# Kernel tuning notes

Measured on AMD Instinct MI355X. Metric: run time of the kernel, lower is better.

Reference implementation:

```python
import jax, jax.numpy as jnp
import numpy as np

DIM = 96
GROUPS = 8          # SPPE factor
CG = DIM // GROUPS  # channels per SPPE group = 12
D_STATE = 16
D_CONV = 4
D_INNER = 2 * DIM   # expand=2
DT_RANK = 6         # ceil(96/16)
EPS = 1e-5


def setup_inputs() -> dict:
    key = jax.random.key(0)
    ks = jax.random.split(key, 16)
    def w(k, shape, s=0.02):
        return (jax.random.normal(k, shape) * s).astype(jnp.float32)
    z = lambda *s: jnp.zeros(s, jnp.float32)
    inp = {
        "x": jax.random.normal(ks[0], (2, DIM, 32, 32, 32), dtype=jnp.float32),
        # SPPE params
        "sppe_c1_w": w(ks[1], (CG, CG)), "sppe_c1_b": z(CG),
        "sppe_c3_w": w(ks[2], (CG, CG, 3, 3, 3)), "sppe_c3_b": z(CG),
        "sppe_gn_w": jnp.ones((CG,), jnp.float32), "sppe_gn_b": z(CG),
        # Mamba params (mamba_ssm defaults: proj biases False, conv bias True)
        "in_proj_w": w(ks[3], (2 * D_INNER, DIM)),
        "conv1d_w": w(ks[4], (D_INNER, D_CONV), 0.1), "conv1d_b": z(D_INNER),
        "x_proj_w": w(ks[5], (DT_RANK + 2 * D_STATE, D_INNER)),
        "dt_proj_w": w(ks[6], (D_INNER, DT_RANK), 0.1),
        "dt_proj_b": w(ks[7], (D_INNER,), 0.1),
        "A_log": jnp.log(jnp.tile(jnp.arange(1, D_STATE + 1, dtype=jnp.float32), (D_INNER, 1))),
        "ssm_D": jnp.ones((D_INNER,), jnp.float32),
        "out_proj_w": w(ks[8], (DIM, D_INNER)),
        # MlpChannel params (1x1 Conv3d == pointwise linear over channels)
        "mlp_fc1_w": w(ks[9], (4 * DIM, DIM)), "mlp_fc1_b": z(4 * DIM),
        "mlp_fc2_w": w(ks[10], (DIM, 4 * DIM)), "mlp_fc2_b": z(DIM),
    }
    return inp


def _inorm(x):
    # InstanceNorm3d (affine=False, biased var) over spatial dims per (b,c)
    m = jnp.mean(x, axis=(2, 3, 4), keepdims=True)
    v = jnp.var(x, axis=(2, 3, 4), keepdims=True)
    return (x - m) * jax.lax.rsqrt(v + EPS)


def _sppe(x, c1_w, c1_b, c3_w, c3_b, gn_w, gn_b):
    b, c, h, w, d = x.shape
    bg = b * GROUPS
    gx = x.reshape(bg, CG, h, w, d)
    # directional pools, each ending as (bg, CG, axis_len, 1, 1)
    x_h = jnp.mean(gx, axis=(3, 4), keepdims=True)                      # (bg,CG,h,1,1)
    x_w = jnp.mean(gx, axis=(2, 4), keepdims=True).transpose(0, 1, 3, 2, 4)
    x_d = jnp.mean(gx, axis=(2, 3), keepdims=True).transpose(0, 1, 4, 3, 2)
    hwd = jnp.concatenate([x_h, x_w, x_d], axis=2)[..., 0, 0]          # (bg,CG,h+w+d)
    hwd = jnp.einsum("oc,bcn->bon", c1_w, hwd) + c1_b[:, None]
    g_h = jax.nn.sigmoid(hwd[:, :, :h])[:, :, :, None, None]           # (bg,CG,h,1,1)
    g_w = jax.nn.sigmoid(hwd[:, :, h:h + w])[:, :, None, :, None]      # (bg,CG,1,w,1)
    g_d = jax.nn.sigmoid(hwd[:, :, h + w:])[:, :, None, None, :]       # (bg,CG,1,1,d)
    gated = gx * g_h * g_w * g_d
    # GroupNorm(num_groups=CG, num_channels=CG) == per-channel norm + affine
    gm = jnp.mean(gated, axis=(2, 3, 4), keepdims=True)
    gv = jnp.var(gated, axis=(2, 3, 4), keepdims=True)
    x1 = (gated - gm) * jax.lax.rsqrt(gv + EPS)
    x1 = x1 * gn_w[:, None, None, None] + gn_b[:, None, None, None]
    x2 = jax.lax.conv_general_dilated(
        gx, c3_w, (1, 1, 1), [(1, 1)] * 3,
        dimension_numbers=("NCDHW", "OIDHW", "NCDHW")) + c3_b[:, None, None, None]
    n = h * w * d
    x11 = jax.nn.softmax(jnp.mean(x1, axis=(2, 3, 4)), axis=-1)        # (bg,CG)
    x21 = jax.nn.softmax(jnp.mean(x2, axis=(2, 3, 4)), axis=-1)
    x12 = x2.reshape(bg, CG, n)
    x22 = x1.reshape(bg, CG, n)
    weights = (jnp.einsum("bc,bcn->bn", x11, x12)
               + jnp.einsum("bc,bcn->bn", x21, x22)).reshape(bg, 1, h, w, d)
    return (gx * jax.nn.sigmoid(weights)).reshape(b, c, h, w, d)


def _mamba(seq, in_proj_w, conv1d_w, conv1d_b, x_proj_w, dt_proj_w, dt_proj_b,
           A_log, ssm_D, out_proj_w):
    # seq: (B, L, DIM)
    B, L, _ = seq.shape
    xz = seq @ in_proj_w.T                       # (B,L,2*E)
    xm, zg = jnp.split(xz, 2, axis=-1)
    # depthwise causal conv1d along L
    xc = jax.lax.conv_general_dilated(
        xm.transpose(0, 2, 1), conv1d_w[:, None, :], (1,), [(D_CONV - 1, 0)],
        dimension_numbers=("NCH", "OIH", "NCH"), feature_group_count=D_INNER)
    xc = jax.nn.silu((xc + conv1d_b[:, None]).transpose(0, 2, 1))  # (B,L,E)
    dbl = xc @ x_proj_w.T                         # (B,L,DT_RANK+2N)
    dt = jax.nn.softplus(dbl[..., :DT_RANK] @ dt_proj_w.T + dt_proj_b)  # (B,L,E)
    Bm = dbl[..., DT_RANK:DT_RANK + D_STATE]      # (B,L,N)
    Cm = dbl[..., DT_RANK + D_STATE:]             # (B,L,N)
    A = -jnp.exp(A_log)                           # (E,N)

    def step(h, t):
        dt_t, b_t, c_t, x_t = t                   # (B,E),(B,N),(B,N),(B,E)
        dA = jnp.exp(dt_t[:, :, None] * A)        # (B,E,N)
        h = h * dA + (dt_t * x_t)[:, :, None] * b_t[:, None, :]
        return h, jnp.einsum("ben,bn->be", h, c_t)

    h0 = jnp.zeros((B, D_INNER, D_STATE), seq.dtype)
    _, ys = jax.lax.scan(step, h0, (dt.transpose(1, 0, 2), Bm.transpose(1, 0, 2),
                                    Cm.transpose(1, 0, 2), xc.transpose(1, 0, 2)))
    y = ys.transpose(1, 0, 2) + xc * ssm_D
    y = y * jax.nn.silu(zg)
    return y @ out_proj_w.T                       # (B,L,DIM)


def reference(x, sppe_c1_w, sppe_c1_b, sppe_c3_w, sppe_c3_b, sppe_gn_w, sppe_gn_b,
              in_proj_w, conv1d_w, conv1d_b, x_proj_w, dt_proj_w, dt_proj_b,
              A_log, ssm_D, out_proj_w, mlp_fc1_w, mlp_fc1_b, mlp_fc2_w, mlp_fc2_b):
    y_sppe = _sppe(x, sppe_c1_w, sppe_c1_b, sppe_c3_w, sppe_c3_b, sppe_gn_w, sppe_gn_b)
    B, C, H, W, Dd = x.shape
    L = H * W * Dd
    seq = _inorm(x).reshape(B, C, L).transpose(0, 2, 1)           # (B,L,C)
    out = _mamba(seq, in_proj_w, conv1d_w, conv1d_b, x_proj_w,
                 dt_proj_w, dt_proj_b, A_log, ssm_D, out_proj_w)
    xo = out.transpose(0, 2, 1).reshape(B, C, H, W, Dd)
    xo = _inorm(xo) * y_sppe
    t = jnp.einsum("oc,bchwd->bohwd", mlp_fc1_w, xo) + mlp_fc1_b[:, None, None, None]
    t = jax.nn.gelu(t, approximate=False)
    t = jnp.einsum("oc,bchwd->bohwd", mlp_fc2_w, t) + mlp_fc2_b[:, None, None, None]
    return t + x
```

## Files before the change

kernel.cpp:

```cpp
#include <hip/hip_runtime.h>
#include <math.h>

#define NSPA 32768
#define TCH 32
#define NCH 1024
#define EPS 1e-5f

#define ST_MEAN   0
#define ST_RSTD   192
#define ST_GM     384
#define ST_GRSTD  576
#define ST_X2SUM  768
#define ST_XH     1024
#define ST_XW     7168
#define ST_XD     13312
#define ST_GATE   19456
#define ST_MEAN2  38400
#define ST_RSTD2  38592
#define ST_WT     40960

__device__ __forceinline__ float sigmoidf_(float x){ return 1.f/(1.f+__expf(-x)); }
__device__ __forceinline__ float siluf_(float x){ return x/(1.f+__expf(-x)); }
__device__ __forceinline__ float geluf_(float x){ return 0.5f*x*(1.f+erff(x*0.70710678118654752f)); }
__device__ __forceinline__ float softplusf_(float x){ return fmaxf(x,0.f) + log1pf(__expf(-fabsf(x))); }

__global__ void k_stats(const float* __restrict__ x, float* __restrict__ st) {
  int bc = blockIdx.x;
  int t = threadIdx.x;
  __shared__ float xh_s[32], xw_s[32], xd_s[32], red[16], red2[16];
  if (t < 32) { xh_s[t]=0.f; xw_s[t]=0.f; xd_s[t]=0.f; }
  __syncthreads();
  const float* px = x + (size_t)bc*NSPA;
  float s=0.f, s2=0.f;
  for (int it=0; it<32; ++it) {
    float v = px[it*1024 + t];
    s += v; s2 += v*v;
    float wv = v;
    #pragma unroll
    for (int m=32;m>=1;m>>=1) wv += __shfl_xor(wv,m);
    if ((t&63)==0) atomicAdd(&xh_s[it], wv);
  }
  atomicAdd(&xw_s[(t>>5)&31], s);
  atomicAdd(&xd_s[t&31], s);
  float rs=s, rs2=s2;
  #pragma unroll
  for (int m=32;m>=1;m>>=1){ rs += __shfl_xor(rs,m); rs2 += __shfl_xor(rs2,m); }
  if ((t&63)==0){ red[t>>6]=rs; red2[t>>6]=rs2; }
  __syncthreads();
  if (t==0){
    float S=0.f,S2=0.f;
    for (int w=0;w<16;w++){ S+=red[w]; S2+=red2[w]; }
    float mn = S/(float)NSPA;
    float var = S2/(float)NSPA - mn*mn;
    st[ST_MEAN+bc] = mn;
    st[ST_RSTD+bc] = rsqrtf(var+EPS);
  }
  if (t<32){
    st[ST_XH + bc*32 + t] = xh_s[t]*(1.f/1024.f);
    st[ST_XW + bc*32 + t] = xw_s[t]*(1.f/1024.f);
    st[ST_XD + bc*32 + t] = xd_s[t]*(1.f/1024.f);
  }
}

__global__ void k_gates(const float* __restrict__ c1w, const float* __restrict__ c1b,
                        float* __restrict__ st) {
  int bg = blockIdx.x; int b = bg>>3; int g = bg&7;
  for (int i = threadIdx.x; i < 12*96; i += 128) {
    int co = i/96, pos = i%96;
    float acc = c1b[co];
    for (int cg=0; cg<12; ++cg) {
      int bc = b*96 + g*12 + cg;
      float hv;
      if (pos < 32)      hv = st[ST_XH + bc*32 + pos];
      else if (pos < 64) hv = st[ST_XW + bc*32 + pos-32];
      else               hv = st[ST_XD + bc*32 + pos-64];
      acc += c1w[co*12+cg]*hv;
    }
    st[ST_GATE + bg*1152 + i] = sigmoidf_(acc);
  }
}

__global__ void k_gated(const float* __restrict__ x, float* __restrict__ gated,
                        float* __restrict__ st) {
  int bc = blockIdx.x; int bg = bc/12; int cg = bc%12;
  int t = threadIdx.x;
  const float* gate = st + ST_GATE + bg*1152 + cg*96;
  float gw = gate[32 + (t>>5)];
  float gd = gate[64 + (t&31)];
  const float* px = x + (size_t)bc*NSPA;
  float* pg = gated + (size_t)bc*NSPA;
  __shared__ float red[16], red2[16];
  float s=0.f, s2=0.f;
  for (int it=0; it<32; ++it) {
    float gh = gate[it];
    float v = px[it*1024+t]*gh*gw*gd;
    pg[it*1024+t] = v;
    s += v; s2 += v*v;
  }
  #pragma unroll
  for (int m=32;m>=1;m>>=1){ s += __shfl_xor(s,m); s2 += __shfl_xor(s2,m); }
  if ((t&63)==0){ red[t>>6]=s; red2[t>>6]=s2; }
  __syncthreads();
  if (t==0){
    float S=0.f,S2=0.f;
    for (int w=0;w<16;w++){ S+=red[w]; S2+=red2[w]; }
    float mn = S/(float)NSPA;
    float var = S2/(float)NSPA - mn*mn;
    st[ST_GM+bc] = mn;
    st[ST_GRSTD+bc] = rsqrtf(var+EPS);
  }
}

__global__ void k_wt(const float* __restrict__ c3w, float* __restrict__ wt) {
  int idx = blockIdx.x*256 + threadIdx.x;
  if (idx >= 3888) return;
  int co = idx/324, r = idx%324;
  wt[r*12 + co] = c3w[co*324 + r];
}

__global__ void k_w1t(const float* __restrict__ W1, float* __restrict__ W1t) {
  int idx = blockIdx.x*256 + threadIdx.x;
  if (idx >= 384*96) return;
  int k = idx/384, h = idx%384;
  W1t[idx] = W1[(size_t)h*96 + k];
}
__global__ void k_w2t(const float* __restrict__ W2, float* __restrict__ W2t) {
  int idx = blockIdx.x*256 + threadIdx.x;
  if (idx >= 384*96) return;
  int k = idx/96, o = idx%96;
  W2t[idx] = W2[(size_t)o*384 + k];
}

__global__ void k_conv3(const float* __restrict__ x, const float* __restrict__ wt,
                        const float* __restrict__ c3b, float* __restrict__ x2,
                        float* __restrict__ st) {
  __shared__ float sl[3][12*324];
  __shared__ float ssum[12];
  int bg = blockIdx.z;
  int w0 = (blockIdx.x & 1)*16, d0 = (blockIdx.x >> 1)*16;
  int h0 = blockIdx.y*4;
  int tid = threadIdx.x;
  if (tid < 12) ssum[tid] = 0.f;

  const float* xb = x + (size_t)bg*12*NSPA;

  auto load_slab = [&](int hh, int s){
    for (int i=tid; i<3888; i+=256){
      int ci = i/324, r = i%324;
      int lw = r/18, ld = r%18;
      int gw = w0-1+lw, gd = d0-1+ld;
      float v = 0.f;
      if ((unsigned)hh<32u && (unsigned)gw<32u && (unsigned)gd<32u)
        v = xb[(size_t)ci*NSPA + hh*1024 + gw*32 + gd];
      sl[s][i] = v;
    }
  };

  load_slab(h0-1, ((h0-1)%3+3)%3);
  load_slab(h0,   h0%3);
  load_slab(h0+1, (h0+1)%3);
  __syncthreads();

  int w = tid>>4, d = tid&15;
  int base_wd = w*18 + d;
  float b0v=c3b[0],b1v=c3b[1],b2v=c3b[2],b3v=c3b[3],b4v=c3b[4],b5v=c3b[5],
        b6v=c3b[6],b7v=c3b[7],b8v=c3b[8],b9v=c3b[9],b10v=c3b[10],b11v=c3b[11];

  for (int it=0; it<4; ++it){
    int h = h0 + it;
    const float* sm1 = sl[((h-1)%3+3)%3];
    const float* s00 = sl[h%3];
    const float* sp1 = sl[(h+1)%3];
    float acc[12];
    acc[0]=b0v; acc[1]=b1v; acc[2]=b2v; acc[3]=b3v; acc[4]=b4v; acc[5]=b5v;
    acc[6]=b6v; acc[7]=b7v; acc[8]=b8v; acc[9]=b9v; acc[10]=b10v; acc[11]=b11v;
    for (int ci=0; ci<12; ++ci){
      const float* w_ci = wt + ci*324;
      #pragma unroll
      for (int kh=0;kh<3;kh++){
        const float* sp = (kh==0)? sm1 : ((kh==1)? s00 : sp1);
        const float* srow = sp + ci*324 + base_wd;
        #pragma unroll
        for (int kw=0;kw<3;kw++){
          #pragma unroll
          for (int kd=0;kd<3;kd++){
            float v = srow[kw*18 + kd];
            const float4* wp = (const float4*)(w_ci + (kh*9+kw*3+kd)*12);
            float4 wa = wp[0], wb = wp[1], wc = wp[2];
            acc[0]=fmaf(wa.x,v,acc[0]); acc[1]=fmaf(wa.y,v,acc[1]);
            acc[2]=fmaf(wa.z,v,acc[2]); acc[3]=fmaf(wa.w,v,acc[3]);
            acc[4]=fmaf(wb.x,v,acc[4]); acc[5]=fmaf(wb.y,v,acc[5]);
            acc[6]=fmaf(wb.z,v,acc[6]); acc[7]=fmaf(wb.w,v,acc[7]);
            acc[8]=fmaf(wc.x,v,acc[8]); acc[9]=fmaf(wc.y,v,acc[9]);
            acc[10]=fmaf(wc.z,v,acc[10]); acc[11]=fmaf(wc.w,v,acc[11]);
          }
        }
      }
    }
    int l = h*1024 + (w0+w)*32 + (d0+d);
    #pragma unroll
    for (int co=0;co<12;co++){
      float r = acc[co];
      x2[(size_t)(bg*12+co)*NSPA + l] = r;
      float rv = r;
      #pragma unroll
      for (int m=32;m>=1;m>>=1) rv += __shfl_xor(rv,m);
      if ((tid&63)==0) atomicAdd(&ssum[co], rv);
    }
    __syncthreads();
    if (it<3){
      load_slab(h+2, (h+2)%3);
      __syncthreads();
    }
  }
  if (tid<12) atomicAdd(&st[ST_X2SUM + bg*12 + tid], ssum[tid]);
}

__global__ void k_sppe_out(const float* __restrict__ x, const float* __restrict__ gated,
                           const float* __restrict__ x2, const float* __restrict__ gnw,
                           const float* __restrict__ gnb, const float* __restrict__ st,
                           float* __restrict__ ysppe) {
  int bg = blockIdx.y; int b = bg>>3; int g = bg&7;
  __shared__ float x11s[12], alphas[12], betasum_s;
  if (threadIdx.x==0){
    float m1=-1e30f, m2=-1e30f;
    float mu2[12];
    for (int cg=0;cg<12;cg++){
      int bc=b*96+g*12+cg;
      mu2[cg] = st[ST_X2SUM+bc]*(1.f/(float)NSPA);
      m1 = fmaxf(m1, gnb[cg]); m2 = fmaxf(m2, mu2[cg]);
    }
    float e1[12], e2[12]; float s1=0.f, s2=0.f;
    for (int cg=0;cg<12;cg++){ e1[cg]=expf(gnb[cg]-m1); s1+=e1[cg];
                               e2[cg]=expf(mu2[cg]-m2); s2+=e2[cg]; }
    float bs=0.f;
    for (int cg=0;cg<12;cg++){
      int bc=b*96+g*12+cg;
      float x11 = e1[cg]/s1;
      float x21 = e2[cg]/s2;
      x11s[cg]=x11;
      float gr = st[ST_GRSTD+bc], gm = st[ST_GM+bc];
      alphas[cg] = x21*gr*gnw[cg];
      bs += x21*(gnb[cg] - gm*gr*gnw[cg]);
    }
    betasum_s = bs;
  }
  __syncthreads();
  int l = blockIdx.x*256 + threadIdx.x;
  float wsum = betasum_s;
  int bc0 = b*96+g*12;
  for (int cg=0;cg<12;cg++){
    size_t off = (size_t)(bc0+cg)*NSPA + l;
    wsum += x11s[cg]*x2[off] + alphas[cg]*gated[off];
  }
  float sig = sigmoidf_(wsum);
  for (int cg=0;cg<12;cg++){
    size_t off = (size_t)(bc0+cg)*NSPA + l;
    ysppe[off] = x[off]*sig;
  }
}

__global__ void k_gemm_in(const float* __restrict__ A, const float* __restrict__ W,
                          float* __restrict__ xm_t, float* __restrict__ zg_t,
                          const float* __restrict__ mean, const float* __restrict__ rstd) {
  __shared__ float As[96*64];
  int b = blockIdx.y; int l0 = blockIdx.x*64; int tid = threadIdx.x;
  for (int i=tid;i<96*64;i+=256){
    int k=i>>6, l=i&63;
    float v = A[((size_t)b*96+k)*NSPA + l0+l];
    As[i] = (v-mean[b*96+k])*rstd[b*96+k];
  }
  __syncthreads();
  int l4=(tid&15)*4; int og=tid>>4;
  for (int o0=og*4; o0<384; o0+=64){
    float acc[16];
    #pragma unroll
    for (int i=0;i<16;i++) acc[i]=0.f;
    for (int k=0;k<96;k++){
      float4 a = *(const float4*)&As[k*64+l4];
      #pragma unroll
      for (int j=0;j<4;j++){
        float wv = W[(size_t)(o0+j)*96+k];
        acc[j*4+0]+=wv*a.x; acc[j*4+1]+=wv*a.y; acc[j*4+2]+=wv*a.z; acc[j*4+3]+=wv*a.w;
      }
    }
    #pragma unroll
    for (int i=0;i<4;i++){
      int l = l0+l4+i;
      float4 r; r.x=acc[0*4+i]; r.y=acc[1*4+i]; r.z=acc[2*4+i]; r.w=acc[3*4+i];
      if (o0 < 192) *(float4*)&xm_t[((size_t)b*NSPA + l)*192 + o0] = r;
      else          *(float4*)&zg_t[((size_t)b*NSPA + l)*192 + (o0-192)] = r;
    }
  }
}

__global__ void k_conv1d_t(const float* __restrict__ xm_t, const float* __restrict__ cw,
                           const float* __restrict__ cb, float* __restrict__ xc_t) {
  int b = blockIdx.y; int l0 = blockIdx.x*64; int e = threadIdx.x;
  float4 w4 = *(const float4*)&cw[e*4];
  float bias = cb[e];
  const float* base = xm_t + (size_t)b*NSPA*192 + e;
  float* out = xc_t + (size_t)b*NSPA*192 + e;
  float hm3 = (l0>0) ? base[(size_t)(l0-3)*192] : 0.f;
  float hm2 = (l0>0) ? base[(size_t)(l0-2)*192] : 0.f;
  float hm1 = (l0>0) ? base[(size_t)(l0-1)*192] : 0.f;
  for (int l=0;l<64;l++){
    float cur = base[(size_t)(l0+l)*192];
    float acc = bias + w4.x*hm3 + w4.y*hm2 + w4.z*hm1 + w4.w*cur;
    out[(size_t)(l0+l)*192] = siluf_(acc);
    hm3=hm2; hm2=hm1; hm1=cur;
  }
}

__global__ void k_gemm_xp(const float* __restrict__ A, const float* __restrict__ W,
                          float* __restrict__ dbl_t) {
  __shared__ float As[192*64];
  int b = blockIdx.y; int l0 = blockIdx.x*64; int tid = threadIdx.x;
  for (int f=tid; f<48*64; f+=256){
    int l = f&63, kq = f>>6;
    float4 v = *(const float4*)&A[((size_t)b*NSPA + l0+l)*192 + kq*4];
    As[(kq*4+0)*64+l]=v.x; As[(kq*4+1)*64+l]=v.y;
    As[(kq*4+2)*64+l]=v.z; As[(kq*4+3)*64+l]=v.w;
  }
  __syncthreads();
  int l4=(tid&15)*4; int og=tid>>4;
  for (int o0=og*4; o0<40; o0+=64){
    float acc[16];
    #pragma unroll
    for (int i=0;i<16;i++) acc[i]=0.f;
    for (int k=0;k<192;k++){
      float4 a = *(const float4*)&As[k*64+l4];
      #pragma unroll
      for (int j=0;j<4;j++){
        int o = o0+j;
        int row = (o<32) ? (o+6) : (o-32);
        float wv = (o<38) ? W[(size_t)row*192+k] : 0.f;
        acc[j*4+0]+=wv*a.x; acc[j*4+1]+=wv*a.y; acc[j*4+2]+=wv*a.z; acc[j*4+3]+=wv*a.w;
      }
    }
    #pragma unroll
    for (int i=0;i<4;i++){
      int l = l0+l4+i;
      float4 r; r.x=acc[0*4+i]; r.y=acc[1*4+i]; r.z=acc[2*4+i]; r.w=acc[3*4+i];
      *(float4*)&dbl_t[((size_t)b*NSPA + l)*40 + o0] = r;
    }
  }
}

__global__ void k_gemm_out(const float* __restrict__ A, const float* __restrict__ W,
                           float* __restrict__ out) {
  __shared__ float As[192*64];
  int b = blockIdx.y; int l0 = blockIdx.x*64; int tid = threadIdx.x;
  for (int f=tid; f<48*64; f+=256){
    int l = f&63, kq = f>>6;
    float4 v = *(const float4*)&A[((size_t)b*NSPA + l0+l)*192 + kq*4];
    As[(kq*4+0)*64+l]=v.x; As[(kq*4+1)*64+l]=v.y;
    As[(kq*4+2)*64+l]=v.z; As[(kq*4+3)*64+l]=v.w;
  }
  __syncthreads();
  int l4=(tid&15)*4; int og=tid>>4;
  for (int o0=og*4; o0<96; o0+=64){
    float acc[16];
    #pragma unroll
    for (int i=0;i<16;i++) acc[i]=0.f;
    for (int k=0;k<192;k++){
      float4 a = *(const float4*)&As[k*64+l4];
      #pragma unroll
      for (int j=0;j<4;j++){
        float wv = W[(size_t)(o0+j)*192+k];
        acc[j*4+0]+=wv*a.x; acc[j*4+1]+=wv*a.y; acc[j*4+2]+=wv*a.z; acc[j*4+3]+=wv*a.w;
      }
    }
    #pragma unroll
    for (int j=0;j<4;j++){
      int o=o0+j;
      float4 r; r.x=acc[j*4+0]; r.y=acc[j*4+1]; r.z=acc[j*4+2]; r.w=acc[j*4+3];
      *(float4*)&out[((size_t)b*96+o)*NSPA + l0+l4] = r;
    }
  }
}

__global__ void k_scanA(const float* __restrict__ xc_t, const float* __restrict__ dbl_t,
                        const float* __restrict__ dtw, const float* __restrict__ dtb,
                        const float* __restrict__ A_log,
                        float* __restrict__ P, float* __restrict__ hend) {
  int b = blockIdx.y, ch = blockIdx.x; int e = threadIdx.x;
  float An[16];
  #pragma unroll
  for (int n=0;n<16;n++) An[n] = -__expf(A_log[e*16+n]);
  float wdt[6];
  #pragma unroll
  for (int j=0;j<6;j++) wdt[j]=dtw[e*6+j];
  float bdt = dtb[e];
  const float* drow = dbl_t + ((size_t)b*NSPA + (size_t)ch*TCH)*40;
  const float* xrow = xc_t + ((size_t)b*NSPA + (size_t)ch*TCH)*192 + e;
  float h[16], Pp[16];
  #pragma unroll
  for (int n=0;n<16;n++){ h[n]=0.f; Pp[n]=1.f; }
  for (int l=0;l<TCH;l++){
    const float* u = drow + l*40;
    float4 b0=*(const float4*)(u+0), b1=*(const float4*)(u+4),
           b2=*(const float4*)(u+8), b3=*(const float4*)(u+12);
    float4 d4=*(const float4*)(u+32);
    float2 d2=*(const float2*)(u+36);
    float x = xrow[(size_t)l*192];
    float pre = bdt + wdt[0]*d4.x + wdt[1]*d4.y + wdt[2]*d4.z
                    + wdt[3]*d4.w + wdt[4]*d2.x + wdt[5]*d2.y;
    float dte = softplusf_(pre);
    float dtx = dte*x;
    float Bv[16] = {b0.x,b0.y,b0.z,b0.w, b1.x,b1.y,b1.z,b1.w,
                    b2.x,b2.y,b2.z,b2.w, b3.x,b3.y,b3.z,b3.w};
    #pragma unroll
    for (int n=0;n<16;n++){
      float a = __expf(dte*An[n]);
      Pp[n] *= a;
      h[n] = h[n]*a + dtx*Bv[n];
    }
  }
  size_t o = (((size_t)b*NCH+ch)*192+e)*16;
  #pragma unroll
  for (int q=0;q<4;q++){
    float4 rp; rp.x=Pp[q*4+0]; rp.y=Pp[q*4+1]; rp.z=Pp[q*4+2]; rp.w=Pp[q*4+3];
    *(float4*)&P[o+q*4] = rp;
    float4 rh; rh.x=h[q*4+0]; rh.y=h[q*4+1]; rh.z=h[q*4+2]; rh.w=h[q*4+3];
    *(float4*)&hend[o+q*4] = rh;
  }
}

__global__ void k_scanB(const float* __restrict__ P, const float* __restrict__ hend,
                        float* __restrict__ Hs) {
  __shared__ float sP[16][64], sH[16][64];
  int b = blockIdx.y;
  int rl = threadIdx.x & 63;
  int cg = threadIdx.x >> 6;
  int r  = blockIdx.x*64 + rl;
  size_t base = (size_t)b*NCH*3072 + r;
  int c0 = cg*64;
  float Pl = 1.f, hl = 0.f;
  for (int c=c0; c<c0+64; ++c){
    size_t idx = base + (size_t)c*3072;
    float Pc = P[idx], Hc = hend[idx];
    hl = fmaf(Pc, hl, Hc);
    Pl *= Pc;
  }
  sP[cg][rl] = Pl; sH[cg][rl] = hl;
  __syncthreads();
  float H = 0.f;
  for (int g=0; g<cg; ++g) H = fmaf(sP[g][rl], H, sH[g][rl]);
  for (int c=c0; c<c0+64; ++c){
    size_t idx = base + (size_t)c*3072;
    float Pc = P[idx], Hc = hend[idx];
    Hs[idx] = H;
    H = fmaf(Pc, H, Hc);
  }
}

__global__ void k_scanC(const float* xc_t, const float* __restrict__ dbl_t,
                        const float* __restrict__ dtw, const float* __restrict__ dtb,
                        const float* __restrict__ A_log, const float* __restrict__ Hs,
                        const float* __restrict__ ssm_D, const float* __restrict__ zg_t,
                        float* y_t) {
  int b = blockIdx.y, ch = blockIdx.x; int e = threadIdx.x;
  float An[16];
  #pragma unroll
  for (int n=0;n<16;n++) An[n] = -__expf(A_log[e*16+n]);
  float wdt[6];
  #pragma unroll
  for (int j=0;j<6;j++) wdt[j]=dtw[e*6+j];
  float bdt = dtb[e];
  float Dv = ssm_D[e];
  const float* drow = dbl_t + ((size_t)b*NSPA + (size_t)ch*TCH)*40;
  const float* xrow = xc_t + ((size_t)b*NSPA + (size_t)ch*TCH)*192 + e;
  const float* zrow = zg_t + ((size_t)b*NSPA + (size_t)ch*TCH)*192 + e;
  float* yrow = y_t + ((size_t)b*NSPA + (size_t)ch*TCH)*192 + e;
  float h[16];
  size_t ho = (((size_t)b*NCH+ch)*192+e)*16;
  #pragma unroll
  for (int q=0;q<4;q++){
    float4 hv = *(const float4*)&Hs[ho+q*4];
    h[q*4+0]=hv.x; h[q*4+1]=hv.y; h[q*4+2]=hv.z; h[q*4+3]=hv.w;
  }
  for (int l=0;l<TCH;l++){
    const float* u = drow + l*40;
    float4 b0=*(const float4*)(u+0), b1=*(const float4*)(u+4),
           b2=*(const float4*)(u+8), b3=*(const float4*)(u+12);
    float4 c0=*(const float4*)(u+16), c1=*(const float4*)(u+20),
           c2=*(const float4*)(u+24), c3=*(const float4*)(u+28);
    float4 d4=*(const float4*)(u+32);
    float2 d2=*(const float2*)(u+36);
    float x = xrow[(size_t)l*192];
    float z = zrow[(size_t)l*192];
    float pre = bdt + wdt[0]*d4.x + wdt[1]*d4.y + wdt[2]*d4.z
                    + wdt[3]*d4.w + wdt[4]*d2.x + wdt[5]*d2.y;
    float dte = softplusf_(pre);
    float dtx = dte*x;
    float Bv[16] = {b0.x,b0.y,b0.z,b0.w, b1.x,b1.y,b1.z,b1.w,
                    b2.x,b2.y,b2.z,b2.w, b3.x,b3.y,b3.z,b3.w};
    float Cv[16] = {c0.x,c0.y,c0.z,c0.w, c1.x,c1.y,c1.z,c1.w,
                    c2.x,c2.y,c2.z,c2.w, c3.x,c3.y,c3.z,c3.w};
    float yp = 0.f;
    #pragma unroll
    for (int n=0;n<16;n++){
      float a = __expf(dte*An[n]);
      h[n] = h[n]*a + dtx*Bv[n];
      yp += h[n]*Cv[n];
    }
    yrow[(size_t)l*192] = (yp + x*Dv)*siluf_(z);
  }
}

__global__ void k_stats2(const float* __restrict__ outb, float* __restrict__ st) {
  int bc = blockIdx.x; int t = threadIdx.x;
  const float* p = outb + (size_t)bc*NSPA;
  float s=0.f, s2=0.f;
  for (int i=t;i<NSPA;i+=256){ float v=p[i]; s+=v; s2+=v*v; }
  __shared__ float red[4], red2[4];
  #pragma unroll
  for (int m=32;m>=1;m>>=1){ s += __shfl_xor(s,m); s2 += __shfl_xor(s2,m); }
  if ((t&63)==0){ red[t>>6]=s; red2[t>>6]=s2; }
  __syncthreads();
  if (t==0){
    float S=red[0]+red[1]+red[2]+red[3];
    float S2=red2[0]+red2[1]+red2[2]+red2[3];
    float mn=S/(float)NSPA; float var=S2/(float)NSPA-mn*mn;
    st[ST_MEAN2+bc]=mn; st[ST_RSTD2+bc]=rsqrtf(var+EPS);
  }
}

__global__ void k_mlpF(const float* __restrict__ outb, const float* __restrict__ ysppe,
                       const float* __restrict__ st,
                       const float* __restrict__ W1t, const float* __restrict__ b1,
                       const float* __restrict__ W2t, const float* __restrict__ b2,
                       const float* __restrict__ x, float* __restrict__ dout) {
  __shared__ float xoS[96*64];
  __shared__ float hidS[32*64];
  int b = blockIdx.y; int l0 = blockIdx.x*64; int tid = threadIdx.x;
  for (int i=tid;i<96*64;i+=256){
    int k=i>>6, l=i&63;
    size_t off = ((size_t)b*96+k)*NSPA + l0+l;
    xoS[i] = (outb[off]-st[ST_MEAN2+b*96+k])*st[ST_RSTD2+b*96+k]*ysppe[off];
  }
  __syncthreads();
  int wv = __builtin_amdgcn_readfirstlane(tid >> 6);
  int lane = tid & 63;
  float acc2[24];
  #pragma unroll
  for (int i=0;i<24;i++) acc2[i]=0.f;
  int o0 = wv*24;

  for (int c=0; c<12; ++c){
    int h0 = c*32 + wv*8;
    float acc1[8];
    #pragma unroll
    for (int i=0;i<8;i++) acc1[i]=0.f;
    for (int k=0;k<96;k++){
      float a = xoS[k*64 + lane];
      const float4* wp = (const float4*)&W1t[(size_t)k*384 + h0];
      float4 w0=wp[0], w1=wp[1];
      acc1[0]=fmaf(w0.x,a,acc1[0]);  acc1[1]=fmaf(w0.y,a,acc1[1]);
      acc1[2]=fmaf(w0.z,a,acc1[2]);  acc1[3]=fmaf(w0.w,a,acc1[3]);
      acc1[4]=fmaf(w1.x,a,acc1[4]);  acc1[5]=fmaf(w1.y,a,acc1[5]);
      acc1[6]=fmaf(w1.z,a,acc1[6]);  acc1[7]=fmaf(w1.w,a,acc1[7]);
    }
    if (c) __syncthreads();
    #pragma unroll
    for (int j=0;j<8;j++)
      hidS[(wv*8+j)*64 + lane] = geluf_(acc1[j] + b1[h0+j]);
    __syncthreads();
    for (int k2=0;k2<32;k2++){
      float a = hidS[k2*64 + lane];
      int kg = c*32 + k2;
      const float4* wp = (const float4*)&W2t[(size_t)kg*96 + o0];
      float4 w0=wp[0], w1=wp[1], w2=wp[2], w3=wp[3], w4=wp[4], w5=wp[5];
      acc2[0]=fmaf(w0.x,a,acc2[0]);  acc2[1]=fmaf(w0.y,a,acc2[1]);
      acc2[2]=fmaf(w0.z,a,acc2[2]);  acc2[3]=fmaf(w0.w,a,acc2[3]);
      acc2[4]=fmaf(w1.x,a,acc2[4]);  acc2[5]=fmaf(w1.y,a,acc2[5]);
      acc2[6]=fmaf(w1.z,a,acc2[6]);  acc2[7]=fmaf(w1.w,a,acc2[7]);
      acc2[8]=fmaf(w2.x,a,acc2[8]);  acc2[9]=fmaf(w2.y,a,acc2[9]);
      acc2[10]=fmaf(w2.z,a,acc2[10]); acc2[11]=fmaf(w2.w,a,acc2[11]);
      acc2[12]=fmaf(w3.x,a,acc2[12]); acc2[13]=fmaf(w3.y,a,acc2[13]);
      acc2[14]=fmaf(w3.z,a,acc2[14]); acc2[15]=fmaf(w3.w,a,acc2[15]);
      acc2[16]=fmaf(w4.x,a,acc2[16]); acc2[17]=fmaf(w4.y,a,acc2[17]);
      acc2[18]=fmaf(w4.z,a,acc2[18]); acc2[19]=fmaf(w4.w,a,acc2[19]);
      acc2[20]=fmaf(w5.x,a,acc2[20]); acc2[21]=fmaf(w5.y,a,acc2[21]);
      acc2[22]=fmaf(w5.z,a,acc2[22]); acc2[23]=fmaf(w5.w,a,acc2[23]);
    }
  }
  #pragma unroll
  for (int j=0;j<24;j++){
    int o = o0 + j;
    size_t off = ((size_t)b*96+o)*NSPA + l0 + lane;
    dout[off] = acc2[j] + b2[o] + x[off];
  }
}

extern "C" void kernel_launch(void* const* d_in, const int* in_sizes, int n_in,
                              void* d_out, int out_size, void* d_ws, size_t ws_size,
                              hipStream_t stream) {
  const float* x        = (const float*)d_in[0];
  const float* c1w      = (const float*)d_in[1];
  const float* c1b      = (const float*)d_in[2];
  const float* c3w      = (const float*)d_in[3];
  const float* c3b      = (const float*)d_in[4];
  const float* gnw      = (const float*)d_in[5];
  const float* gnb      = (const float*)d_in[6];
  const float* in_proj  = (const float*)d_in[7];
  const float* conv1dw  = (const float*)d_in[8];
  const float* conv1db  = (const float*)d_in[9];
  const float* xprojw   = (const float*)d_in[10];
  const float* dtw      = (const float*)d_in[11];
  const float* dtb      = (const float*)d_in[12];
  const float* A_log    = (const float*)d_in[13];
  const float* ssm_D    = (const float*)d_in[14];
  const float* outprojw = (const float*)d_in[15];
  const float* W1       = (const float*)d_in[16];
  const float* b1       = (const float*)d_in[17];
  const float* W2       = (const float*)d_in[18];
  const float* b2       = (const float*)d_in[19];
  float* dout = (float*)d_out;

  float* ws = (float*)d_ws;
  const size_t o_st = 0;
  const size_t o_A  = 65536;
  const size_t o_B  = o_A + 12582912;
  const size_t o_C  = o_B + 12582912;
  const size_t o_D  = o_C + 12582912;
  const size_t o_E  = o_D + 6291456;
  const size_t o_F  = o_E + 6291456;
  float* st    = ws + o_st;
  float* xm_t  = ws + o_A;
  float* P     = ws + o_A;
  float* Hs    = ws + o_A + 6291456;
  float* zg_t  = ws + o_B;
  float* xc_t  = ws + o_C;
  float* y_t   = ws + o_C;
  float* gated = ws + o_D;
  float* dbl_t = ws + o_D;
  float* W1t   = ws + o_D + 3000000;
  float* W2t   = ws + o_D + 3100000;
  float* x2b   = ws + o_E;
  float* hendb = ws + o_E;
  float* outb  = ws + o_E;
  float* ysppe = ws + o_F;
  float* wtb   = st + ST_WT;

  hipMemsetAsync(st, 0, 65536*sizeof(float), stream);

  k_stats<<<192, 1024, 0, stream>>>(x, st);
  k_gates<<<16, 128, 0, stream>>>(c1w, c1b, st);
  k_gated<<<192, 1024, 0, stream>>>(x, gated, st);
  k_wt<<<16, 256, 0, stream>>>(c3w, wtb);
  k_conv3<<<dim3(4,8,16), 256, 0, stream>>>(x, wtb, c3b, x2b, st);
  k_sppe_out<<<dim3(128,16), 256, 0, stream>>>(x, gated, x2b, gnw, gnb, st, ysppe);
  k_gemm_in<<<dim3(512,2), 256, 0, stream>>>(x, in_proj, xm_t, zg_t,
                                             st+ST_MEAN, st+ST_RSTD);
  k_conv1d_t<<<dim3(512,2), 192, 0, stream>>>(xm_t, conv1dw, conv1db, xc_t);
  k_w1t<<<144, 256, 0, stream>>>(W1, W1t);
  k_w2t<<<144, 256, 0, stream>>>(W2, W2t);
  k_gemm_xp<<<dim3(512,2), 256, 0, stream>>>(xc_t, xprojw, dbl_t);
  k_scanA<<<dim3(NCH,2), 192, 0, stream>>>(xc_t, dbl_t, dtw, dtb, A_log, P, hendb);
  k_scanB<<<dim3(48,2), 1024, 0, stream>>>(P, hendb, Hs);
  k_scanC<<<dim3(NCH,2), 192, 0, stream>>>(xc_t, dbl_t, dtw, dtb, A_log, Hs,
                                           ssm_D, zg_t, y_t);
  k_gemm_out<<<dim3(512,2), 256, 0, stream>>>(y_t, outprojw, outb);
  k_stats2<<<192, 256, 0, stream>>>(outb, st);
  k_mlpF<<<dim3(512,2), 256, 0, stream>>>(outb, ysppe, st, W1t, b1, W2t, b2, x, dout);
}
```

Measured before the change: 888.3 us.

## Fuse in_proj with conv1d, store SPPE sigmoid only, fold stats into out_proj

Merges the three weight-transpose kernels into one prep kernel and pre-transposes the in_proj, x_proj and out_proj weights. Fuses the in_proj GEMM with the causal depthwise conv1d and SiLU, recomputing a 3-token halo so the xm_t intermediate is never written. The SPPE output becomes a per-group sigmoid map that the MLP kernel multiplies with x, and out_proj accumulates the instance-norm statistics through atomics so the separate stats pass goes away. The MLP hidden buffer is double-buffered to drop one barrier per chunk. These changes cut global memory traffic and launches, at the cost of redundant halo dot products and atomic contention.

```diff
diff --git a/kernel.cpp b/kernel.cpp
--- a/kernel.cpp
+++ b/kernel.cpp
@@ -17,12 +17,44 @@
 #define ST_GATE   19456
 #define ST_MEAN2  38400
 #define ST_RSTD2  38592
+#define ST_OSUM   38784
+#define ST_OSQ    38976
 #define ST_WT     40960
 
 __device__ __forceinline__ float sigmoidf_(float x){ return 1.f/(1.f+__expf(-x)); }
 __device__ __forceinline__ float siluf_(float x){ return x/(1.f+__expf(-x)); }
 __device__ __forceinline__ float geluf_(float x){ return 0.5f*x*(1.f+erff(x*0.70710678118654752f)); }
 __device__ __forceinline__ float softplusf_(float x){ return fmaxf(x,0.f) + log1pf(__expf(-fabsf(x))); }
+
+__global__ void k_prep(const float* __restrict__ c3w, const float* __restrict__ W1,
+                       const float* __restrict__ W2, const float* __restrict__ Wip,
+                       const float* __restrict__ xpw, const float* __restrict__ Wout,
+                       float* __restrict__ wt, float* __restrict__ W1t,
+                       float* __restrict__ W2t, float* __restrict__ Wipt,
+                       float* __restrict__ xpWt, float* __restrict__ Wot) {
+  int idx = blockIdx.x*256 + threadIdx.x;
+  if (idx < 3888) {
+    int co = idx/324, r = idx%324;
+    wt[r*12+co] = c3w[co*324+r];
+  } else if (idx < 40752) {
+    int i = idx-3888; int k = i/384, h = i%384;
+    W1t[i] = W1[(size_t)h*96+k];
+  } else if (idx < 77616) {
+    int i = idx-40752; int k = i/96, o = i%96;
+    W2t[i] = W2[(size_t)o*384+k];
+  } else if (idx < 114480) {
+    int i = idx-77616; int k = i/384, r = i%384;
+    Wipt[i] = Wip[(size_t)r*96+k];
+  } else if (idx < 123696) {
+    int i = idx-114480; int e = i/48, o = i%48;
+    float v = 0.f;
+    if (o < 38) { int row = (o<32)? (o+6) : (o-32); v = xpw[(size_t)row*192+e]; }
+    xpWt[i] = v;
+  } else if (idx < 142128) {
+    int i = idx-123696; int e = i/96, o = i%96;
+    Wot[i] = Wout[(size_t)o*192+e];
+  }
+}
 
 __global__ void k_stats(const float* __restrict__ x, float* __restrict__ st) {
   int bc = blockIdx.x;
@@ -109,26 +141,6 @@
     st[ST_GM+bc] = mn;
     st[ST_GRSTD+bc] = rsqrtf(var+EPS);
   }
-}
-
-__global__ void k_wt(const float* __restrict__ c3w, float* __restrict__ wt) {
-  int idx = blockIdx.x*256 + threadIdx.x;
-  if (idx >= 3888) return;
-  int co = idx/324, r = idx%324;
-  wt[r*12 + co] = c3w[co*324 + r];
-}
-
-__global__ void k_w1t(const float* __restrict__ W1, float* __restrict__ W1t) {
-  int idx = blockIdx.x*256 + threadIdx.x;
-  if (idx >= 384*96) return;
-  int k = idx/384, h = idx%384;
-  W1t[idx] = W1[(size_t)h*96 + k];
-}
-__global__ void k_w2t(const float* __restrict__ W2, float* __restrict__ W2t) {
-  int idx = blockIdx.x*256 + threadIdx.x;
-  if (idx >= 384*96) return;
-  int k = idx/96, o = idx%96;
-  W2t[idx] = W2[(size_t)o*384 + k];
 }
 
 __global__ void k_conv3(const float* __restrict__ x, const float* __restrict__ wt,
@@ -216,10 +228,10 @@
   if (tid<12) atomicAdd(&st[ST_X2SUM + bg*12 + tid], ssum[tid]);
 }
 
-__global__ void k_sppe_out(const float* __restrict__ x, const float* __restrict__ gated,
+__global__ void k_sppe_out(const float* __restrict__ gated,
                            const float* __restrict__ x2, const float* __restrict__ gnw,
                            const float* __restrict__ gnb, const float* __restrict__ st,
-                           float* __restrict__ ysppe) {
+                           float* __restrict__ sigb) {
   int bg = blockIdx.y; int b = bg>>3; int g = bg&7;
   __shared__ float x11s[12], alphas[12], betasum_s;
   if (threadIdx.x==0){
@@ -253,131 +265,193 @@
     size_t off = (size_t)(bc0+cg)*NSPA + l;
     wsum += x11s[cg]*x2[off] + alphas[cg]*gated[off];
   }
-  float sig = sigmoidf_(wsum);
-  for (int cg=0;cg<12;cg++){
-    size_t off = (size_t)(bc0+cg)*NSPA + l;
-    ysppe[off] = x[off]*sig;
-  }
-}
-
-__global__ void k_gemm_in(const float* __restrict__ A, const float* __restrict__ W,
-                          float* __restrict__ xm_t, float* __restrict__ zg_t,
-                          const float* __restrict__ mean, const float* __restrict__ rstd) {
+  sigb[(size_t)bg*NSPA + l] = sigmoidf_(wsum);
+}
+
+__global__ void k_front(const float* __restrict__ x, const float* __restrict__ Wipt,
+                        const float* __restrict__ Wip,
+                        const float* __restrict__ cw, const float* __restrict__ cb,
+                        const float* __restrict__ st,
+                        float* __restrict__ xc_t, float* __restrict__ zg_t) {
   __shared__ float As[96*64];
+  __shared__ float outS[48*65];
+  __shared__ float haloS[3*192];
   int b = blockIdx.y; int l0 = blockIdx.x*64; int tid = threadIdx.x;
+  const float* mean = st + ST_MEAN + b*96;
+  const float* rstd = st + ST_RSTD + b*96;
   for (int i=tid;i<96*64;i+=256){
     int k=i>>6, l=i&63;
-    float v = A[((size_t)b*96+k)*NSPA + l0+l];
-    As[i] = (v-mean[b*96+k])*rstd[b*96+k];
-  }
-  __syncthreads();
-  int l4=(tid&15)*4; int og=tid>>4;
-  for (int o0=og*4; o0<384; o0+=64){
-    float acc[16];
+    As[i] = (x[((size_t)b*96+k)*NSPA + l0+l]-mean[k])*rstd[k];
+  }
+  for (int i=tid;i<576;i+=256){
+    int j=i/192, e=i%192;
+    int t = l0-3+j;
+    float s = 0.f;
+    if (t >= 0){
+      const float* wr = Wip + (size_t)e*96;
+      for (int k=0;k<96;k++)
+        s += wr[k]*(x[((size_t)b*96+k)*NSPA + t]-mean[k])*rstd[k];
+    }
+    haloS[i] = s;
+  }
+  __syncthreads();
+  int wv = __builtin_amdgcn_readfirstlane(tid>>6);
+  int lane = tid&63;
+  for (int p=0;p<8;++p){
+    int r0 = p*48 + wv*12;
+    float acc[12];
     #pragma unroll
-    for (int i=0;i<16;i++) acc[i]=0.f;
+    for (int j=0;j<12;j++) acc[j]=0.f;
     for (int k=0;k<96;k++){
-      float4 a = *(const float4*)&As[k*64+l4];
+      float a = As[k*64+lane];
+      const float4* wp = (const float4*)&Wipt[(size_t)k*384 + r0];
+      float4 w0=wp[0],w1=wp[1],w2=wp[2];
+      acc[0]=fmaf(w0.x,a,acc[0]);  acc[1]=fmaf(w0.y,a,acc[1]);
+      acc[2]=fmaf(w0.z,a,acc[2]);  acc[3]=fmaf(w0.w,a,acc[3]);
+      acc[4]=fmaf(w1.x,a,acc[4]);  acc[5]=fmaf(w1.y,a,acc[5]);
+      acc[6]=fmaf(w1.z,a,acc[6]);  acc[7]=fmaf(w1.w,a,acc[7]);
+      acc[8]=fmaf(w2.x,a,acc[8]);  acc[9]=fmaf(w2.y,a,acc[9]);
+      acc[10]=fmaf(w2.z,a,acc[10]); acc[11]=fmaf(w2.w,a,acc[11]);
+    }
+    if (p) __syncthreads();
+    if (p < 4){
       #pragma unroll
-      for (int j=0;j<4;j++){
-        float wv = W[(size_t)(o0+j)*96+k];
-        acc[j*4+0]+=wv*a.x; acc[j*4+1]+=wv*a.y; acc[j*4+2]+=wv*a.z; acc[j*4+3]+=wv*a.w;
+      for (int j=0;j<12;j++){
+        int e = r0 + j;
+        float v = acc[j];
+        float vm1 = __shfl_up(v,1);
+        float vm2 = __shfl_up(v,2);
+        float vm3 = __shfl_up(v,3);
+        if (lane==0) vm1 = haloS[2*192+e];
+        if (lane<=1) vm2 = haloS[(1+lane)*192+e];
+        if (lane<=2) vm3 = haloS[(0+lane)*192+e];
+        float4 w4 = *(const float4*)&cw[e*4];
+        float r_ = cb[e] + w4.x*vm3 + w4.y*vm2 + w4.z*vm1 + w4.w*v;
+        outS[(wv*12+j)*65 + lane] = siluf_(r_);
       }
-    }
+    } else {
+      #pragma unroll
+      for (int j=0;j<12;j++) outS[(wv*12+j)*65 + lane] = acc[j];
+    }
+    __syncthreads();
+    float* dst = (p<4) ? xc_t : zg_t;
+    int e0 = (p<4) ? p*48 : (p-4)*48;
+    for (int i=tid; i<64*12; i+=256){
+      int l = i/12, q = i%12;
+      float4 v;
+      v.x = outS[(q*4+0)*65 + l];
+      v.y = outS[(q*4+1)*65 + l];
+      v.z = outS[(q*4+2)*65 + l];
+      v.w = outS[(q*4+3)*65 + l];
+      *(float4*)&dst[((size_t)b*NSPA + l0+l)*192 + e0 + q*4] = v;
+    }
+  }
+}
+
+__global__ void k_gemm_xp(const float* __restrict__ A, const float* __restrict__ xpWt,
+                          float* __restrict__ dbl_t) {
+  __shared__ float As[96*65];
+  __shared__ float dblS[48*65];
+  int b = blockIdx.y; int l0 = blockIdx.x*64; int tid = threadIdx.x;
+  int wv = __builtin_amdgcn_readfirstlane(tid>>6);
+  int lane = tid&63;
+  int o0 = wv*12;
+  float acc[12];
+  #pragma unroll
+  for (int j=0;j<12;j++) acc[j]=0.f;
+  for (int h=0;h<2;++h){
+    if (h) __syncthreads();
+    for (int i=tid;i<64*24;i+=256){
+      int l=i/24, q=i%24;
+      float4 v = *(const float4*)&A[((size_t)b*NSPA + l0+l)*192 + h*96 + q*4];
+      As[(q*4+0)*65+l]=v.x; As[(q*4+1)*65+l]=v.y;
+      As[(q*4+2)*65+l]=v.z; As[(q*4+3)*65+l]=v.w;
+    }
+    __syncthreads();
+    for (int k=0;k<96;k++){
+      float a = As[k*65+lane];
+      const float4* wp = (const float4*)&xpWt[(size_t)(h*96+k)*48 + o0];
+      float4 w0=wp[0],w1=wp[1],w2=wp[2];
+      acc[0]=fmaf(w0.x,a,acc[0]);  acc[1]=fmaf(w0.y,a,acc[1]);
+      acc[2]=fmaf(w0.z,a,acc[2]);  acc[3]=fmaf(w0.w,a,acc[3]);
+      acc[4]=fmaf(w1.x,a,acc[4]);  acc[5]=fmaf(w1.y,a,acc[5]);
+      acc[6]=fmaf(w1.z,a,acc[6]);  acc[7]=fmaf(w1.w,a,acc[7]);
+      acc[8]=fmaf(w2.x,a,acc[8]);  acc[9]=fmaf(w2.y,a,acc[9]);
+      acc[10]=fmaf(w2.z,a,acc[10]); acc[11]=fmaf(w2.w,a,acc[11]);
+    }
+  }
+  __syncthreads();
+  #pragma unroll
+  for (int j=0;j<12;j++) dblS[(o0+j)*65 + lane] = acc[j];
+  __syncthreads();
+  for (int i=tid;i<64*10;i+=256){
+    int l=i/10, q=i%10;
+    float4 v;
+    v.x = dblS[(q*4+0)*65+l]; v.y = dblS[(q*4+1)*65+l];
+    v.z = dblS[(q*4+2)*65+l]; v.w = dblS[(q*4+3)*65+l];
+    *(float4*)&dbl_t[((size_t)b*NSPA + l0+l)*40 + q*4] = v;
+  }
+}
+
+__global__ void k_gemm_out(const float* __restrict__ A, const float* __restrict__ Wot,
+                           float* __restrict__ out, float* __restrict__ st) {
+  __shared__ float As[96*65];
+  int b = blockIdx.y; int l0 = blockIdx.x*64; int tid = threadIdx.x;
+  int wv = __builtin_amdgcn_readfirstlane(tid>>6);
+  int lane = tid&63;
+  int o0 = wv*24;
+  float acc[24];
+  #pragma unroll
+  for (int j=0;j<24;j++) acc[j]=0.f;
+  for (int h=0;h<2;++h){
+    if (h) __syncthreads();
+    for (int i=tid;i<64*24;i+=256){
+      int l=i/24, q=i%24;
+      float4 v = *(const float4*)&A[((size_t)b*NSPA + l0+l)*192 + h*96 + q*4];
+      As[(q*4+0)*65+l]=v.x; As[(q*4+1)*65+l]=v.y;
+      As[(q*4+2)*65+l]=v.z; As[(q*4+3)*65+l]=v.w;
+    }
+    __syncthreads();
+    for (int k=0;k<96;k++){
+      float a = As[k*65+lane];
+      const float4* wp = (const float4*)&Wot[(size_t)(h*96+k)*96 + o0];
+      float4 w0=wp[0],w1=wp[1],w2=wp[2],w3=wp[3],w4=wp[4],w5=wp[5];
+      acc[0]=fmaf(w0.x,a,acc[0]);  acc[1]=fmaf(w0.y,a,acc[1]);
+      acc[2]=fmaf(w0.z,a,acc[2]);  acc[3]=fmaf(w0.w,a,acc[3]);
+      acc[4]=fmaf(w1.x,a,acc[4]);  acc[5]=fmaf(w1.y,a,acc[5]);
+      acc[6]=fmaf(w1.z,a,acc[6]);  acc[7]=fmaf(w1.w,a,acc[7]);
+      acc[8]=fmaf(w2.x,a,acc[8]);  acc[9]=fmaf(w2.y,a,acc[9]);
+      acc[10]=fmaf(w2.z,a,acc[10]); acc[11]=fmaf(w2.w,a,acc[11]);
+      acc[12]=fmaf(w3.x,a,acc[12]); acc[13]=fmaf(w3.y,a,acc[13]);
+      acc[14]=fmaf(w3.z,a,acc[14]); acc[15]=fmaf(w3.w,a,acc[15]);
+      acc[16]=fmaf(w4.x,a,acc[16]); acc[17]=fmaf(w4.y,a,acc[17]);
+      acc[18]=fmaf(w4.z,a,acc[18]); acc[19]=fmaf(w4.w,a,acc[19]);
+      acc[20]=fmaf(w5.x,a,acc[20]); acc[21]=fmaf(w5.y,a,acc[21]);
+      acc[22]=fmaf(w5.z,a,acc[22]); acc[23]=fmaf(w5.w,a,acc[23]);
+    }
+  }
+  #pragma unroll
+  for (int j=0;j<24;j++){
+    out[((size_t)b*96 + o0+j)*NSPA + l0 + lane] = acc[j];
+  }
+  #pragma unroll
+  for (int j=0;j<24;j++){
+    float s = acc[j], s2 = acc[j]*acc[j];
     #pragma unroll
-    for (int i=0;i<4;i++){
-      int l = l0+l4+i;
-      float4 r; r.x=acc[0*4+i]; r.y=acc[1*4+i]; r.z=acc[2*4+i]; r.w=acc[3*4+i];
-      if (o0 < 192) *(float4*)&xm_t[((size_t)b*NSPA + l)*192 + o0] = r;
-      else          *(float4*)&zg_t[((size_t)b*NSPA + l)*192 + (o0-192)] = r;
-    }
-  }
-}
-
-__global__ void k_conv1d_t(const float* __restrict__ xm_t, const float* __restrict__ cw,
-                           const float* __restrict__ cb, float* __restrict__ xc_t) {
-  int b = blockIdx.y; int l0 = blockIdx.x*64; int e = threadIdx.x;
-  float4 w4 = *(const float4*)&cw[e*4];
-  float bias = cb[e];
-  const float* base = xm_t + (size_t)b*NSPA*192 + e;
-  float* out = xc_t + (size_t)b*NSPA*192 + e;
-  float hm3 = (l0>0) ? base[(size_t)(l0-3)*192] : 0.f;
-  float hm2 = (l0>0) ? base[(size_t)(l0-2)*192] : 0.f;
-  float hm1 = (l0>0) ? base[(size_t)(l0-1)*192] : 0.f;
-  for (int l=0;l<64;l++){
-    float cur = base[(size_t)(l0+l)*192];
-    float acc = bias + w4.x*hm3 + w4.y*hm2 + w4.z*hm1 + w4.w*cur;
-    out[(size_t)(l0+l)*192] = siluf_(acc);
-    hm3=hm2; hm2=hm1; hm1=cur;
-  }
-}
-
-__global__ void k_gemm_xp(const float* __restrict__ A, const float* __restrict__ W,
-                          float* __restrict__ dbl_t) {
-  __shared__ float As[192*64];
-  int b = blockIdx.y; int l0 = blockIdx.x*64; int tid = threadIdx.x;
-  for (int f=tid; f<48*64; f+=256){
-    int l = f&63, kq = f>>6;
-    float4 v = *(const float4*)&A[((size_t)b*NSPA + l0+l)*192 + kq*4];
-    As[(kq*4+0)*64+l]=v.x; As[(kq*4+1)*64+l]=v.y;
-    As[(kq*4+2)*64+l]=v.z; As[(kq*4+3)*64+l]=v.w;
-  }
-  __syncthreads();
-  int l4=(tid&15)*4; int og=tid>>4;
-  for (int o0=og*4; o0<40; o0+=64){
-    float acc[16];
-    #pragma unroll
-    for (int i=0;i<16;i++) acc[i]=0.f;
-    for (int k=0;k<192;k++){
-      float4 a = *(const float4*)&As[k*64+l4];
-      #pragma unroll
-      for (int j=0;j<4;j++){
-        int o = o0+j;
-        int row = (o<32) ? (o+6) : (o-32);
-        float wv = (o<38) ? W[(size_t)row*192+k] : 0.f;
-        acc[j*4+0]+=wv*a.x; acc[j*4+1]+=wv*a.y; acc[j*4+2]+=wv*a.z; acc[j*4+3]+=wv*a.w;
-      }
-    }
-    #pragma unroll
-    for (int i=0;i<4;i++){
-      int l = l0+l4+i;
-      float4 r; r.x=acc[0*4+i]; r.y=acc[1*4+i]; r.z=acc[2*4+i]; r.w=acc[3*4+i];
-      *(float4*)&dbl_t[((size_t)b*NSPA + l)*40 + o0] = r;
-    }
-  }
-}
-
-__global__ void k_gemm_out(const float* __restrict__ A, const float* __restrict__ W,
-                           float* __restrict__ out) {
-  __shared__ float As[192*64];
-  int b = blockIdx.y; int l0 = blockIdx.x*64; int tid = threadIdx.x;
-  for (int f=tid; f<48*64; f+=256){
-    int l = f&63, kq = f>>6;
-    float4 v = *(const float4*)&A[((size_t)b*NSPA + l0+l)*192 + kq*4];
-    As[(kq*4+0)*64+l]=v.x; As[(kq*4+1)*64+l]=v.y;
-    As[(kq*4+2)*64+l]=v.z; As[(kq*4+3)*64+l]=v.w;
-  }
-  __syncthreads();
-  int l4=(tid&15)*4; int og=tid>>4;
-  for (int o0=og*4; o0<96; o0+=64){
-    float acc[16];
-    #pragma unroll
-    for (int i=0;i<16;i++) acc[i]=0.f;
-    for (int k=0;k<192;k++){
-      float4 a = *(const float4*)&As[k*64+l4];
-      #pragma unroll
-      for (int j=0;j<4;j++){
-        float wv = W[(size_t)(o0+j)*192+k];
-        acc[j*4+0]+=wv*a.x; acc[j*4+1]+=wv*a.y; acc[j*4+2]+=wv*a.z; acc[j*4+3]+=wv*a.w;
-      }
-    }
-    #pragma unroll
-    for (int j=0;j<4;j++){
-      int o=o0+j;
-      float4 r; r.x=acc[j*4+0]; r.y=acc[j*4+1]; r.z=acc[j*4+2]; r.w=acc[j*4+3];
-      *(float4*)&out[((size_t)b*96+o)*NSPA + l0+l4] = r;
-    }
-  }
+    for (int m=32;m>=1;m>>=1){ s += __shfl_xor(s,m); s2 += __shfl_xor(s2,m); }
+    if (lane==0){
+      atomicAdd(&st[ST_OSUM + b*96 + o0+j], s);
+      atomicAdd(&st[ST_OSQ  + b*96 + o0+j], s2);
+    }
+  }
+}
+
+__global__ void k_fin(float* __restrict__ st){
+  int t = threadIdx.x;
+  float mn = st[ST_OSUM+t]*(1.f/(float)NSPA);
+  float var = st[ST_OSQ+t]*(1.f/(float)NSPA) - mn*mn;
+  st[ST_MEAN2+t] = mn;
+  st[ST_RSTD2+t] = rsqrtf(var+EPS);
 }
 
 __global__ void k_scanA(const float* __restrict__ xc_t, const float* __restrict__ dbl_t,
@@ -509,36 +583,19 @@
   }
 }
 
-__global__ void k_stats2(const float* __restrict__ outb, float* __restrict__ st) {
-  int bc = blockIdx.x; int t = threadIdx.x;
-  const float* p = outb + (size_t)bc*NSPA;
-  float s=0.f, s2=0.f;
-  for (int i=t;i<NSPA;i+=256){ float v=p[i]; s+=v; s2+=v*v; }
-  __shared__ float red[4], red2[4];
-  #pragma unroll
-  for (int m=32;m>=1;m>>=1){ s += __shfl_xor(s,m); s2 += __shfl_xor(s2,m); }
-  if ((t&63)==0){ red[t>>6]=s; red2[t>>6]=s2; }
-  __syncthreads();
-  if (t==0){
-    float S=red[0]+red[1]+red[2]+red[3];
-    float S2=red2[0]+red2[1]+red2[2]+red2[3];
-    float mn=S/(float)NSPA; float var=S2/(float)NSPA-mn*mn;
-    st[ST_MEAN2+bc]=mn; st[ST_RSTD2+bc]=rsqrtf(var+EPS);
-  }
-}
-
-__global__ void k_mlpF(const float* __restrict__ outb, const float* __restrict__ ysppe,
+__global__ void k_mlpF(const float* __restrict__ outb, const float* __restrict__ sigb,
                        const float* __restrict__ st,
                        const float* __restrict__ W1t, const float* __restrict__ b1,
                        const float* __restrict__ W2t, const float* __restrict__ b2,
                        const float* __restrict__ x, float* __restrict__ dout) {
   __shared__ float xoS[96*64];
-  __shared__ float hidS[32*64];
+  __shared__ float hidS[2][32*64];
   int b = blockIdx.y; int l0 = blockIdx.x*64; int tid = threadIdx.x;
   for (int i=tid;i<96*64;i+=256){
     int k=i>>6, l=i&63;
     size_t off = ((size_t)b*96+k)*NSPA + l0+l;
-    xoS[i] = (outb[off]-st[ST_MEAN2+b*96+k])*st[ST_RSTD2+b*96+k]*ysppe[off];
+    float sv = sigb[((size_t)(b*8 + k/12))*NSPA + l0+l];
+    xoS[i] = (outb[off]-st[ST_MEAN2+b*96+k])*st[ST_RSTD2+b*96+k]*x[off]*sv;
   }
   __syncthreads();
   int wv = __builtin_amdgcn_readfirstlane(tid >> 6);
@@ -562,13 +619,13 @@
       acc1[4]=fmaf(w1.x,a,acc1[4]);  acc1[5]=fmaf(w1.y,a,acc1[5]);
       acc1[6]=fmaf(w1.z,a,acc1[6]);  acc1[7]=fmaf(w1.w,a,acc1[7]);
     }
-    if (c) __syncthreads();
+    float* hb = hidS[c&1];
     #pragma unroll
     for (int j=0;j<8;j++)
-      hidS[(wv*8+j)*64 + lane] = geluf_(acc1[j] + b1[h0+j]);
+      hb[(wv*8+j)*64 + lane] = geluf_(acc1[j] + b1[h0+j]);
     __syncthreads();
     for (int k2=0;k2<32;k2++){
-      float a = hidS[k2*64 + lane];
+      float a = hb[k2*64 + lane];
       int kg = c*32 + k2;
       const float4* wp = (const float4*)&W2t[(size_t)kg*96 + o0];
       float4 w0=wp[0], w1=wp[1], w2=wp[2], w3=wp[3], w4=wp[4], w5=wp[5];
@@ -628,7 +685,6 @@
   const size_t o_E  = o_D + 6291456;
   const size_t o_F  = o_E + 6291456;
   float* st    = ws + o_st;
-  float* xm_t  = ws + o_A;
   float* P     = ws + o_A;
   float* Hs    = ws + o_A + 6291456;
   float* zg_t  = ws + o_B;
@@ -636,33 +692,34 @@
   float* y_t   = ws + o_C;
   float* gated = ws + o_D;
   float* dbl_t = ws + o_D;
-  float* W1t   = ws + o_D + 3000000;
-  float* W2t   = ws + o_D + 3100000;
   float* x2b   = ws + o_E;
   float* hendb = ws + o_E;
   float* outb  = ws + o_E;
-  float* ysppe = ws + o_F;
+  float* W1t   = ws + o_F + 0;
+  float* W2t   = ws + o_F + 40960;
+  float* Wipt  = ws + o_F + 81920;
+  float* xpWt  = ws + o_F + 122880;
+  float* Wot   = ws + o_F + 135168;
+  float* sigb  = ws + o_F + 200704;
   float* wtb   = st + ST_WT;
 
   hipMemsetAsync(st, 0, 65536*sizeof(float), stream);
 
+  k_prep<<<556, 256, 0, stream>>>(c3w, W1, W2, in_proj, xprojw, outprojw,
+                                  wtb, W1t, W2t, Wipt, xpWt, Wot);
   k_stats<<<192, 1024, 0, stream>>>(x, st);
   k_gates<<<16, 128, 0, stream>>>(c1w, c1b, st);
   k_gated<<<192, 1024, 0, stream>>>(x, gated, st);
-  k_wt<<<16, 256, 0, stream>>>(c3w, wtb);
   k_conv3<<<dim3(4,8,16), 256, 0, stream>>>(x, wtb, c3b, x2b, st);
-  k_sppe_out<<<dim3(128,16), 256, 0, stream>>>(x, gated, x2b, gnw, gnb, st, ysppe);
-  k_gemm_in<<<dim3(512,2), 256, 0, stream>>>(x, in_proj, xm_t, zg_t,
-                                             st+ST_MEAN, st+ST_RSTD);
-  k_conv1d_t<<<dim3(512,2), 192, 0, stream>>>(xm_t, conv1dw, conv1db, xc_t);
-  k_w1t<<<144, 256, 0, stream>>>(W1, W1t);
-  k_w2t<<<144, 256, 0, stream>>>(W2, W2t);
-  k_gemm_xp<<<dim3(512,2), 256, 0, stream>>>(xc_t, xprojw, dbl_t);
+  k_sppe_out<<<dim3(128,16), 256, 0, stream>>>(gated, x2b, gnw, gnb, st, sigb);
+  k_front<<<dim3(512,2), 256, 0, stream>>>(x, Wipt, in_proj, conv1dw, conv1db,
+                                           st, xc_t, zg_t);
+  k_gemm_xp<<<dim3(512,2), 256, 0, stream>>>(xc_t, xpWt, dbl_t);
   k_scanA<<<dim3(NCH,2), 192, 0, stream>>>(xc_t, dbl_t, dtw, dtb, A_log, P, hendb);
   k_scanB<<<dim3(48,2), 1024, 0, stream>>>(P, hendb, Hs);
   k_scanC<<<dim3(NCH,2), 192, 0, stream>>>(xc_t, dbl_t, dtw, dtb, A_log, Hs,
                                            ssm_D, zg_t, y_t);
-  k_gemm_out<<<dim3(512,2), 256, 0, stream>>>(y_t, outprojw, outb);
-  k_stats2<<<192, 256, 0, stream>>>(outb, st);
-  k_mlpF<<<dim3(512,2), 256, 0, stream>>>(outb, ysppe, st, W1t, b1, W2t, b2, x, dout);
-}
+  k_gemm_out<<<dim3(512,2), 256, 0, stream>>>(y_t, Wot, outb, st);
+  k_fin<<<1, 192, 0, stream>>>(st);
+  k_mlpF<<<dim3(512,2), 256, 0, stream>>>(outb, sigb, st, W1t, b1, W2t, b2, x, dout);
+}
```

New measurement: 1.074 ms. 21.0% more time.
